# Optimization experiments

Measured on AMD Instinct MI355X. Metric: run time of the kernel, lower is better.

Reference implementation:

```python
import jax, jax.numpy as jnp
import numpy as np

# --- config constants (match init_kwargs) ---
TOP_K = 2          # num_experts_per_token
N_GROUP = 4        # num_expert_group
TOPK_GROUP = 2     # groups selected per token
SCALE = 2.5        # routed_scaling_factor
B, S, D = 2, 2048, 1024
E, F = 8, 512      # num_experts, moe_intermediate_size
SH = 1024          # shared intermediate = moe_intermediate_size * num_shared_experts


def setup_inputs() -> dict:
    key = jax.random.key(0)
    ks = jax.random.split(key, 10)
    w = 0.02
    return {
        "hidden_states": jax.random.normal(ks[0], (B, S, D), jnp.float32),
        "gate_w": jax.random.normal(ks[1], (E, D), jnp.float32) * w,
        "gate_bias": jax.random.normal(ks[2], (E,), jnp.float32) * 0.01,
        "w1": jax.random.normal(ks[3], (E, F, D), jnp.float32) * w,
        "w2": jax.random.normal(ks[4], (E, D, F), jnp.float32) * w,
        "w3": jax.random.normal(ks[5], (E, F, D), jnp.float32) * w,
        "shared_gate_w": jax.random.normal(ks[6], (SH, D), jnp.float32) * w,
        "shared_up_w": jax.random.normal(ks[7], (SH, D), jnp.float32) * w,
        "shared_down_w": jax.random.normal(ks[8], (D, SH), jnp.float32) * w,
    }


def _moe_gate(x2d, gate_w, gate_bias):
    """DeepSeek-V3 style group-limited sigmoid gate (inference path)."""
    T = x2d.shape[0]
    logits = x2d.astype(jnp.float32) @ gate_w.T.astype(jnp.float32)  # [T,E]
    scores = jax.nn.sigmoid(logits)
    sc = scores + gate_bias[None, :]                                  # e_score_correction_bias
    grp = sc.reshape(T, N_GROUP, E // N_GROUP)
    group_scores = jax.lax.top_k(grp, 2)[0].sum(-1)                   # [T,G] sum of top-2 in group
    gidx = jax.lax.top_k(group_scores, TOPK_GROUP)[1]                 # [T,topk_group]
    gmask = jnp.zeros((T, N_GROUP), sc.dtype).at[jnp.arange(T)[:, None], gidx].set(1.0)
    smask = jnp.repeat(gmask, E // N_GROUP, axis=1)                   # [T,E]
    tmp = jnp.where(smask > 0, sc, 0.0)                               # masked_fill(~mask, 0)
    tidx = jax.lax.top_k(tmp, TOP_K)[1]                               # [T,top_k]
    tw = jnp.take_along_axis(scores, tidx, axis=1)                    # weights from unbiased scores
    tw = tw / (tw.sum(-1, keepdims=True) + 1e-20)                     # moe_renormalize
    return tidx, tw * SCALE


def reference(hidden_states, gate_w, gate_bias, w1, w2, w3,
              shared_gate_w, shared_up_w, shared_down_w):
    b, s, d = hidden_states.shape
    x = hidden_states.reshape(-1, d)                                  # [T,D]
    T = x.shape[0]
    tidx, tw = _moe_gate(x, gate_w, gate_bias)
    # dense combine weights: ew[t,e] = sum_k tw[t,k] * (tidx[t,k]==e)
    ew = jnp.zeros((T, E), x.dtype).at[jnp.arange(T)[:, None], tidx].add(tw.astype(x.dtype))
    # routed experts (SwiGLU), computed per expert and combined with ew
    h = jax.nn.silu(jnp.einsum('td,efd->tef', x, w1)) * jnp.einsum('td,efd->tef', x, w3)
    y = jnp.einsum('tef,edf,te->td', h, w2, ew)
    # shared experts applied to identity
    shared = (jax.nn.silu(x @ shared_gate_w.T) * (x @ shared_up_w.T)) @ shared_down_w.T
    return (y + shared).reshape(b, s, d)
```

## Files before the change

kernel.cpp:

```cpp
#include <hip/hip_runtime.h>
#include <hip/hip_bf16.h>
#include <stdint.h>

#define T_TOK 4096
#define D_DIM 1024
#define E_NUM 8
#define F_DIM 512
#define SH_DIM 1024
#define SCALE_F 2.5f

#define BM 128
#define BN 128
#define BK 32
#define LDT 40

#define NBIG (E_NUM * F_DIM * D_DIM)
#define NSML (SH_DIM * D_DIM)
#define NCONV_CHUNKS ((3 * NBIG + 3 * NSML) / 4)
#define MAX_TILES 72

typedef unsigned short ushort_t;
typedef __attribute__((ext_vector_type(8))) short short8;
typedef __attribute__((ext_vector_type(4))) short short4v;
typedef __attribute__((ext_vector_type(4))) float f32x4;

__device__ inline ushort_t f2bf(float f) {
  union { float f; unsigned u; } cv; cv.f = f;
  unsigned u = cv.u;
  unsigned r = (u + 0x7FFFu + ((u >> 16) & 1u)) >> 16;
  return (ushort_t)r;
}

__global__ void gate_kernel(const float* __restrict__ x, const float* __restrict__ gw,
                            const float* __restrict__ gb, float* __restrict__ ew,
                            ushort_t* __restrict__ xb) {
  int t = blockIdx.x;
  int lane = threadIdx.x;
  const float* xr = x + (size_t)t * D_DIM;
  float xv[16];
#pragma unroll
  for (int i = 0; i < 16; i++) xv[i] = xr[lane + (i << 6)];
#pragma unroll
  for (int i = 0; i < 16; i++) xb[(size_t)t * D_DIM + lane + (i << 6)] = f2bf(xv[i]);
  float logit[E_NUM];
#pragma unroll
  for (int e = 0; e < E_NUM; e++) {
    const float* wr = gw + (size_t)e * D_DIM;
    float s = 0.f;
#pragma unroll
    for (int i = 0; i < 16; i++) s += xv[i] * wr[lane + (i << 6)];
#pragma unroll
    for (int off = 32; off; off >>= 1) s += __shfl_xor(s, off, 64);
    logit[e] = s;
  }
  if (lane == 0) {
    float scores[E_NUM], sc[E_NUM];
#pragma unroll
    for (int e = 0; e < E_NUM; e++) {
      scores[e] = 1.f / (1.f + expf(-logit[e]));
      sc[e] = scores[e] + gb[e];
    }
    float gs[4];
#pragma unroll
    for (int g = 0; g < 4; g++) gs[g] = sc[2 * g] + sc[2 * g + 1];
    int g0 = 0;
#pragma unroll
    for (int g = 1; g < 4; g++) if (gs[g] > gs[g0]) g0 = g;
    int g1 = -1;
#pragma unroll
    for (int g = 0; g < 4; g++) { if (g == g0) continue; if (g1 < 0 || gs[g] > gs[g1]) g1 = g; }
    float tmp[E_NUM];
#pragma unroll
    for (int e = 0; e < E_NUM; e++) {
      int g = e >> 1;
      tmp[e] = (g == g0 || g == g1) ? sc[e] : 0.f;
    }
    int e0 = 0;
#pragma unroll
    for (int e = 1; e < E_NUM; e++) if (tmp[e] > tmp[e0]) e0 = e;
    int e1 = -1;
#pragma unroll
    for (int e = 0; e < E_NUM; e++) { if (e == e0) continue; if (e1 < 0 || tmp[e] > tmp[e1]) e1 = e; }
    float w0 = scores[e0], w1v = scores[e1];
    float inv = SCALE_F / (w0 + w1v + 1e-20f);
    float o[E_NUM];
#pragma unroll
    for (int e = 0; e < E_NUM; e++) o[e] = 0.f;
    o[e0] = w0 * inv;
    o[e1] = w1v * inv;
#pragma unroll
    for (int e = 0; e < E_NUM; e++) ew[t * E_NUM + e] = o[e];
  }
}

__global__ void convert_kernel(const float* __restrict__ w1, const float* __restrict__ w2,
                               const float* __restrict__ w3, const float* __restrict__ sg,
                               const float* __restrict__ su, const float* __restrict__ sd,
                               ushort_t* __restrict__ w1b, ushort_t* __restrict__ w2b,
                               ushort_t* __restrict__ w3b, ushort_t* __restrict__ sgb,
                               ushort_t* __restrict__ sub, ushort_t* __restrict__ sdb) {
  size_t chunk = (size_t)blockIdx.x * blockDim.x + threadIdx.x;
  if (chunk >= (size_t)NCONV_CHUNKS) return;
  size_t idx = chunk * 4;
  const float* src; ushort_t* dst;
  if (idx < (size_t)NBIG)                    { src = w1; dst = w1b; }
  else if (idx < 2ull * NBIG)                { src = w2; dst = w2b; idx -= (size_t)NBIG; }
  else if (idx < 3ull * NBIG)                { src = w3; dst = w3b; idx -= 2ull * NBIG; }
  else if (idx < 3ull * NBIG + NSML)         { src = sg; dst = sgb; idx -= 3ull * NBIG; }
  else if (idx < 3ull * NBIG + 2ull * NSML)  { src = su; dst = sub; idx -= 3ull * NBIG + NSML; }
  else                                       { src = sd; dst = sdb; idx -= 3ull * NBIG + 2ull * NSML; }
  f32x4 v = *(const f32x4*)&src[idx];
  short4v o;
  o[0] = (short)f2bf(v[0]); o[1] = (short)f2bf(v[1]);
  o[2] = (short)f2bf(v[2]); o[3] = (short)f2bf(v[3]);
  *(short4v*)&dst[idx] = o;
}

__global__ void build_lists(const float* __restrict__ ew, int* __restrict__ counts,
                            int* __restrict__ toklist) {
  int t = blockIdx.x * blockDim.x + threadIdx.x;
  if (t >= T_TOK) return;
#pragma unroll
  for (int e = 0; e < E_NUM; e++) {
    if (ew[t * E_NUM + e] > 0.f) {
      int p = atomicAdd(&counts[e], 1);
      toklist[e * T_TOK + p] = t;
    }
  }
}

__global__ void assign_kernel(const int* __restrict__ counts, int4* __restrict__ assign,
                              int* __restrict__ meta) {
  if (threadIdx.x != 0 || blockIdx.x != 0) return;
  int total = 0, base = 0;
  for (int e = 0; e < E_NUM; e++) {
    int c = counts[e];
    int nt = (c + BM - 1) / BM;
    for (int i = 0; i < nt; i++) {
      assign[total] = make_int4(e, i, base, c);
      total++;
    }
    base += nt * BM;
  }
  meta[0] = total;
}

__global__ __launch_bounds__(256, 2)
void shared_gemm1(const ushort_t* __restrict__ xb, const ushort_t* __restrict__ gwb,
                  const ushort_t* __restrict__ uwb, ushort_t* __restrict__ hout) {
  __shared__ short la[BM * LDT], lb1[BN * LDT], lb2[BN * LDT];
  int tid = threadIdx.x, wid = tid >> 6, lane = tid & 63;
  int m0 = blockIdx.x * BM, n0 = blockIdx.y * BN;
  int wm = (wid >> 1) << 6, wn = (wid & 1) << 6;
  f32x4 acc1[4][4] = {{{0.f}}}, acc2[4][4] = {{{0.f}}};
  for (int k0 = 0; k0 < D_DIM; k0 += BK) {
#pragma unroll
    for (int i = tid; i < BM * 4; i += 256) {
      int r = i >> 2, c = (i & 3) << 3;
      *(short8*)&la[r * LDT + c]  = *(const short8*)&xb[(size_t)(m0 + r) * D_DIM + k0 + c];
      *(short8*)&lb1[r * LDT + c] = *(const short8*)&gwb[(size_t)(n0 + r) * D_DIM + k0 + c];
      *(short8*)&lb2[r * LDT + c] = *(const short8*)&uwb[(size_t)(n0 + r) * D_DIM + k0 + c];
    }
    __syncthreads();
    int rsel = lane & 15, ksel = (lane >> 4) << 3;
    short8 af[4], bf1[4], bf2[4];
#pragma unroll
    for (int i = 0; i < 4; i++) {
      af[i]  = *(const short8*)&la[(wm + i * 16 + rsel) * LDT + ksel];
      bf1[i] = *(const short8*)&lb1[(wn + i * 16 + rsel) * LDT + ksel];
      bf2[i] = *(const short8*)&lb2[(wn + i * 16 + rsel) * LDT + ksel];
    }
#pragma unroll
    for (int mi = 0; mi < 4; mi++)
#pragma unroll
      for (int ni = 0; ni < 4; ni++) {
        acc1[mi][ni] = __builtin_amdgcn_mfma_f32_16x16x32_bf16(af[mi], bf1[ni], acc1[mi][ni], 0, 0, 0);
        acc2[mi][ni] = __builtin_amdgcn_mfma_f32_16x16x32_bf16(af[mi], bf2[ni], acc2[mi][ni], 0, 0, 0);
      }
    __syncthreads();
  }
  int cw = lane & 15, rw = (lane >> 4) << 2;
#pragma unroll
  for (int mi = 0; mi < 4; mi++)
#pragma unroll
    for (int ni = 0; ni < 4; ni++)
#pragma unroll
      for (int r = 0; r < 4; r++) {
        int row = m0 + wm + mi * 16 + rw + r;
        int col = n0 + wn + ni * 16 + cw;
        float g = acc1[mi][ni][r], u = acc2[mi][ni][r];
        float h = g * (1.f / (1.f + __expf(-g))) * u;
        hout[(size_t)row * SH_DIM + col] = f2bf(h);
      }
}

__global__ __launch_bounds__(256, 2)
void shared_gemm2(const ushort_t* __restrict__ hb, const ushort_t* __restrict__ dwb,
                  float* __restrict__ out) {
  __shared__ short la[BM * LDT], lb[BN * LDT];
  int tid = threadIdx.x, wid = tid >> 6, lane = tid & 63;
  int m0 = blockIdx.x * BM, n0 = blockIdx.y * BN;
  int wm = (wid >> 1) << 6, wn = (wid & 1) << 6;
  f32x4 acc[4][4] = {{{0.f}}};
  for (int k0 = 0; k0 < SH_DIM; k0 += BK) {
#pragma unroll
    for (int i = tid; i < BM * 4; i += 256) {
      int r = i >> 2, c = (i & 3) << 3;
      *(short8*)&la[r * LDT + c] = *(const short8*)&hb[(size_t)(m0 + r) * SH_DIM + k0 + c];
      *(short8*)&lb[r * LDT + c] = *(const short8*)&dwb[(size_t)(n0 + r) * SH_DIM + k0 + c];
    }
    __syncthreads();
    int rsel = lane & 15, ksel = (lane >> 4) << 3;
    short8 af[4], bf[4];
#pragma unroll
    for (int i = 0; i < 4; i++) {
      af[i] = *(const short8*)&la[(wm + i * 16 + rsel) * LDT + ksel];
      bf[i] = *(const short8*)&lb[(wn + i * 16 + rsel) * LDT + ksel];
    }
#pragma unroll
    for (int mi = 0; mi < 4; mi++)
#pragma unroll
      for (int ni = 0; ni < 4; ni++)
        acc[mi][ni] = __builtin_amdgcn_mfma_f32_16x16x32_bf16(af[mi], bf[ni], acc[mi][ni], 0, 0, 0);
    __syncthreads();
  }
  int cw = lane & 15, rw = (lane >> 4) << 2;
#pragma unroll
  for (int mi = 0; mi < 4; mi++)
#pragma unroll
    for (int ni = 0; ni < 4; ni++)
#pragma unroll
      for (int r = 0; r < 4; r++) {
        int row = m0 + wm + mi * 16 + rw + r;
        int col = n0 + wn + ni * 16 + cw;
        out[(size_t)row * D_DIM + col] = acc[mi][ni][r];
      }
}

__global__ __launch_bounds__(256, 2)
void routed_gemm1(const ushort_t* __restrict__ xb, const ushort_t* __restrict__ w1b,
                  const ushort_t* __restrict__ w3b, const int* __restrict__ toklist,
                  const int4* __restrict__ assign, const int* __restrict__ meta,
                  ushort_t* __restrict__ hbuf) {
  if ((int)blockIdx.x >= meta[0]) return;
  int4 as = assign[blockIdx.x];
  int e = as.x, tile = as.y, sbase = as.z, cnt = as.w;
  int n0 = blockIdx.y * BN;
  __shared__ short la[BM * LDT], lb1[BN * LDT], lb2[BN * LDT];
  __shared__ int ttok[BM];
  int tid = threadIdx.x, wid = tid >> 6, lane = tid & 63;
  if (tid < BM) {
    int idx = tile * BM + tid;
    ttok[tid] = (idx < cnt) ? toklist[e * T_TOK + idx] : -1;
  }
  __syncthreads();
  int wm = (wid >> 1) << 6, wn = (wid & 1) << 6;
  f32x4 acc1[4][4] = {{{0.f}}}, acc2[4][4] = {{{0.f}}};
  for (int k0 = 0; k0 < D_DIM; k0 += BK) {
#pragma unroll
    for (int i = tid; i < BM * 4; i += 256) {
      int r = i >> 2, c = (i & 3) << 3;
      int tk = ttok[r];
      short8 va = {};
      if (tk >= 0) va = *(const short8*)&xb[(size_t)tk * D_DIM + k0 + c];
      *(short8*)&la[r * LDT + c] = va;
      *(short8*)&lb1[r * LDT + c] = *(const short8*)&w1b[((size_t)e * F_DIM + n0 + r) * D_DIM + k0 + c];
      *(short8*)&lb2[r * LDT + c] = *(const short8*)&w3b[((size_t)e * F_DIM + n0 + r) * D_DIM + k0 + c];
    }
    __syncthreads();
    int rsel = lane & 15, ksel = (lane >> 4) << 3;
    short8 af[4], bf1[4], bf2[4];
#pragma unroll
    for (int i = 0; i < 4; i++) {
      af[i]  = *(const short8*)&la[(wm + i * 16 + rsel) * LDT + ksel];
      bf1[i] = *(const short8*)&lb1[(wn + i * 16 + rsel) * LDT + ksel];
      bf2[i] = *(const short8*)&lb2[(wn + i * 16 + rsel) * LDT + ksel];
    }
#pragma unroll
    for (int mi = 0; mi < 4; mi++)
#pragma unroll
      for (int ni = 0; ni < 4; ni++) {
        acc1[mi][ni] = __builtin_amdgcn_mfma_f32_16x16x32_bf16(af[mi], bf1[ni], acc1[mi][ni], 0, 0, 0);
        acc2[mi][ni] = __builtin_amdgcn_mfma_f32_16x16x32_bf16(af[mi], bf2[ni], acc2[mi][ni], 0, 0, 0);
      }
    __syncthreads();
  }
  int cw = lane & 15, rw = (lane >> 4) << 2;
#pragma unroll
  for (int mi = 0; mi < 4; mi++)
#pragma unroll
    for (int ni = 0; ni < 4; ni++)
#pragma unroll
      for (int r = 0; r < 4; r++) {
        int lrow = wm + mi * 16 + rw + r;
        int col = n0 + wn + ni * 16 + cw;
        float g = acc1[mi][ni][r], u = acc2[mi][ni][r];
        float h = g * (1.f / (1.f + __expf(-g))) * u;
        hbuf[(size_t)(sbase + tile * BM + lrow) * F_DIM + col] = f2bf(h);
      }
}

__global__ __launch_bounds__(256, 2)
void routed_gemm2(const ushort_t* __restrict__ hbuf, const ushort_t* __restrict__ w2b,
                  const int* __restrict__ toklist, const float* __restrict__ ew,
                  const int4* __restrict__ assign, const int* __restrict__ meta,
                  float* __restrict__ out) {
  if ((int)blockIdx.x >= meta[0]) return;
  int4 as = assign[blockIdx.x];
  int e = as.x, tile = as.y, sbase = as.z, cnt = as.w;
  int n0 = blockIdx.y * BN;
  __shared__ short la[BM * LDT], lb[BN * LDT];
  __shared__ int ttok[BM];
  __shared__ float twt[BM];
  int tid = threadIdx.x, wid = tid >> 6, lane = tid & 63;
  if (tid < BM) {
    int idx = tile * BM + tid;
    int tk = (idx < cnt) ? toklist[e * T_TOK + idx] : -1;
    ttok[tid] = tk;
    twt[tid] = (tk >= 0) ? ew[tk * E_NUM + e] : 0.f;
  }
  __syncthreads();
  int wm = (wid >> 1) << 6, wn = (wid & 1) << 6;
  f32x4 acc[4][4] = {{{0.f}}};
  for (int k0 = 0; k0 < F_DIM; k0 += BK) {
#pragma unroll
    for (int i = tid; i < BM * 4; i += 256) {
      int r = i >> 2, c = (i & 3) << 3;
      *(short8*)&la[r * LDT + c] = *(const short8*)&hbuf[(size_t)(sbase + tile * BM + r) * F_DIM + k0 + c];
      *(short8*)&lb[r * LDT + c] = *(const short8*)&w2b[((size_t)e * D_DIM + n0 + r) * F_DIM + k0 + c];
    }
    __syncthreads();
    int rsel = lane & 15, ksel = (lane >> 4) << 3;
    short8 af[4], bf[4];
#pragma unroll
    for (int i = 0; i < 4; i++) {
      af[i] = *(const short8*)&la[(wm + i * 16 + rsel) * LDT + ksel];
      bf[i] = *(const short8*)&lb[(wn + i * 16 + rsel) * LDT + ksel];
    }
#pragma unroll
    for (int mi = 0; mi < 4; mi++)
#pragma unroll
      for (int ni = 0; ni < 4; ni++)
        acc[mi][ni] = __builtin_amdgcn_mfma_f32_16x16x32_bf16(af[mi], bf[ni], acc[mi][ni], 0, 0, 0);
    __syncthreads();
  }
  int cw = lane & 15, rw = (lane >> 4) << 2;
#pragma unroll
  for (int mi = 0; mi < 4; mi++)
#pragma unroll
    for (int ni = 0; ni < 4; ni++)
#pragma unroll
      for (int r = 0; r < 4; r++) {
        int lrow = wm + mi * 16 + rw + r;
        int tk = ttok[lrow];
        if (tk >= 0) {
          int col = n0 + wn + ni * 16 + cw;
          atomicAdd(&out[(size_t)tk * D_DIM + col], twt[lrow] * acc[mi][ni][r]);
        }
      }
}

extern "C" void kernel_launch(void* const* d_in, const int* in_sizes, int n_in,
                              void* d_out, int out_size, void* d_ws, size_t ws_size,
                              hipStream_t stream) {
  const float* x  = (const float*)d_in[0];
  const float* gw = (const float*)d_in[1];
  const float* gb = (const float*)d_in[2];
  const float* w1 = (const float*)d_in[3];
  const float* w2 = (const float*)d_in[4];
  const float* w3 = (const float*)d_in[5];
  const float* sg = (const float*)d_in[6];
  const float* su = (const float*)d_in[7];
  const float* sd = (const float*)d_in[8];
  float* out = (float*)d_out;

  char* ws = (char*)d_ws;
  size_t off = 0;
  auto alloc = [&](size_t bytes) {
    char* p = ws + off;
    off += (bytes + 255) & ~(size_t)255;
    return p;
  };
  ushort_t* xb   = (ushort_t*)alloc((size_t)T_TOK * D_DIM * 2);
  ushort_t* w1b  = (ushort_t*)alloc((size_t)NBIG * 2);
  ushort_t* w2b  = (ushort_t*)alloc((size_t)NBIG * 2);
  ushort_t* w3b  = (ushort_t*)alloc((size_t)NBIG * 2);
  ushort_t* sgb  = (ushort_t*)alloc((size_t)NSML * 2);
  ushort_t* sub  = (ushort_t*)alloc((size_t)NSML * 2);
  ushort_t* sdb  = (ushort_t*)alloc((size_t)NSML * 2);
  float*    ew   = (float*)alloc((size_t)T_TOK * E_NUM * 4);
  ushort_t* hsh  = (ushort_t*)alloc((size_t)T_TOK * SH_DIM * 2);
  ushort_t* hbuf = (ushort_t*)alloc((size_t)MAX_TILES * BM * F_DIM * 2);
  int*      toklist = (int*)alloc((size_t)E_NUM * T_TOK * 4);
  int*      counts  = (int*)alloc(64);
  int4*     assign  = (int4*)alloc((MAX_TILES + 8) * sizeof(int4));
  int*      meta    = (int*)alloc(64);

  hipMemsetAsync(counts, 0, 64, stream);
  gate_kernel<<<T_TOK, 64, 0, stream>>>(x, gw, gb, ew, xb);
  convert_kernel<<<NCONV_CHUNKS / 256, 256, 0, stream>>>(w1, w2, w3, sg, su, sd,
                                                         w1b, w2b, w3b, sgb, sub, sdb);
  build_lists<<<(T_TOK + 255) / 256, 256, 0, stream>>>(ew, counts, toklist);
  assign_kernel<<<1, 64, 0, stream>>>(counts, assign, meta);
  shared_gemm1<<<dim3(T_TOK / BM, SH_DIM / BN), 256, 0, stream>>>(xb, sgb, sub, hsh);
  shared_gemm2<<<dim3(T_TOK / BM, D_DIM / BN), 256, 0, stream>>>(hsh, sdb, out);
  routed_gemm1<<<dim3(MAX_TILES, F_DIM / BN), 256, 0, stream>>>(xb, w1b, w3b, toklist,
                                                                assign, meta, hbuf);
  routed_gemm2<<<dim3(MAX_TILES, D_DIM / BN), 256, 0, stream>>>(hbuf, w2b, toklist, ew,
                                                                assign, meta, out);
}
```

Baseline: 310.8 us.

## Merge shared and routed expert GEMMs into grouped up and down launches

Combines the shared-expert and routed-expert up-projection GEMMs into one launch, and likewise the two down-projection GEMMs, with block IDs split between the shared and routed work. This lets shared and routed tiles run together on the GPU, filling compute units that the small routed grid left idle and removing launch gaps. Since both kinds of block now accumulate into the output, the output is zeroed with a memset and the shared path goes through the weighted accumulate epilogue, which adds extra memory traffic and atomics.

```diff
diff --git a/kernel.cpp b/kernel.cpp
--- a/kernel.cpp
+++ b/kernel.cpp
@@ -18,6 +18,11 @@
 #define NSML (SH_DIM * D_DIM)
 #define NCONV_CHUNKS ((3 * NBIG + 3 * NSML) / 4)
 #define MAX_TILES 72
+
+#define UP_SHARED_BLOCKS 256
+#define UP_TOTAL (UP_SHARED_BLOCKS + MAX_TILES * 4)
+#define DN_SHARED_BLOCKS 256
+#define DN_TOTAL (DN_SHARED_BLOCKS + MAX_TILES * 8)
 
 typedef unsigned short ushort_t;
 typedef __attribute__((ext_vector_type(8))) short short8;
@@ -146,20 +151,58 @@
 }
 
 __global__ __launch_bounds__(256, 2)
-void shared_gemm1(const ushort_t* __restrict__ xb, const ushort_t* __restrict__ gwb,
-                  const ushort_t* __restrict__ uwb, ushort_t* __restrict__ hout) {
+void up_gemm(const ushort_t* __restrict__ xb,
+             const ushort_t* __restrict__ sgb, const ushort_t* __restrict__ sub,
+             const ushort_t* __restrict__ w1b, const ushort_t* __restrict__ w3b,
+             const int* __restrict__ toklist,
+             const int4* __restrict__ assign, const int* __restrict__ meta,
+             ushort_t* __restrict__ hsh, ushort_t* __restrict__ hbuf) {
   __shared__ short la[BM * LDT], lb1[BN * LDT], lb2[BN * LDT];
+  __shared__ int ttok[BM];
+  int bid = blockIdx.x;
   int tid = threadIdx.x, wid = tid >> 6, lane = tid & 63;
-  int m0 = blockIdx.x * BM, n0 = blockIdx.y * BN;
+
+  const ushort_t *b1base, *b2base;
+  ushort_t* dst;
+  int n0, dstride;
+  size_t rowbase;
+
+  if (bid < UP_SHARED_BLOCKS) {
+    int m0 = (bid >> 3) * BM;
+    n0 = (bid & 7) * BN;
+    b1base = sgb + (size_t)n0 * D_DIM;
+    b2base = sub + (size_t)n0 * D_DIM;
+    dst = hsh; dstride = SH_DIM; rowbase = m0;
+    if (tid < BM) ttok[tid] = m0 + tid;
+  } else {
+    int rid = bid - UP_SHARED_BLOCKS;
+    int tidx = rid >> 2;
+    if (tidx >= meta[0]) return;
+    int4 as = assign[tidx];
+    int e = as.x, tile = as.y, sbase = as.z, cnt = as.w;
+    n0 = (rid & 3) * BN;
+    b1base = w1b + ((size_t)e * F_DIM + n0) * D_DIM;
+    b2base = w3b + ((size_t)e * F_DIM + n0) * D_DIM;
+    dst = hbuf; dstride = F_DIM; rowbase = (size_t)sbase + (size_t)tile * BM;
+    if (tid < BM) {
+      int idx = tile * BM + tid;
+      ttok[tid] = (idx < cnt) ? toklist[e * T_TOK + idx] : -1;
+    }
+  }
+  __syncthreads();
+
   int wm = (wid >> 1) << 6, wn = (wid & 1) << 6;
   f32x4 acc1[4][4] = {{{0.f}}}, acc2[4][4] = {{{0.f}}};
   for (int k0 = 0; k0 < D_DIM; k0 += BK) {
 #pragma unroll
     for (int i = tid; i < BM * 4; i += 256) {
       int r = i >> 2, c = (i & 3) << 3;
-      *(short8*)&la[r * LDT + c]  = *(const short8*)&xb[(size_t)(m0 + r) * D_DIM + k0 + c];
-      *(short8*)&lb1[r * LDT + c] = *(const short8*)&gwb[(size_t)(n0 + r) * D_DIM + k0 + c];
-      *(short8*)&lb2[r * LDT + c] = *(const short8*)&uwb[(size_t)(n0 + r) * D_DIM + k0 + c];
+      int tk = ttok[r];
+      short8 va = {};
+      if (tk >= 0) va = *(const short8*)&xb[(size_t)tk * D_DIM + k0 + c];
+      *(short8*)&la[r * LDT + c]  = va;
+      *(short8*)&lb1[r * LDT + c] = *(const short8*)&b1base[(size_t)r * D_DIM + k0 + c];
+      *(short8*)&lb2[r * LDT + c] = *(const short8*)&b2base[(size_t)r * D_DIM + k0 + c];
     }
     __syncthreads();
     int rsel = lane & 15, ksel = (lane >> 4) << 3;
@@ -186,148 +229,63 @@
     for (int ni = 0; ni < 4; ni++)
 #pragma unroll
       for (int r = 0; r < 4; r++) {
-        int row = m0 + wm + mi * 16 + rw + r;
-        int col = n0 + wn + ni * 16 + cw;
-        float g = acc1[mi][ni][r], u = acc2[mi][ni][r];
-        float h = g * (1.f / (1.f + __expf(-g))) * u;
-        hout[(size_t)row * SH_DIM + col] = f2bf(h);
-      }
-}
-
-__global__ __launch_bounds__(256, 2)
-void shared_gemm2(const ushort_t* __restrict__ hb, const ushort_t* __restrict__ dwb,
-                  float* __restrict__ out) {
-  __shared__ short la[BM * LDT], lb[BN * LDT];
-  int tid = threadIdx.x, wid = tid >> 6, lane = tid & 63;
-  int m0 = blockIdx.x * BM, n0 = blockIdx.y * BN;
-  int wm = (wid >> 1) << 6, wn = (wid & 1) << 6;
-  f32x4 acc[4][4] = {{{0.f}}};
-  for (int k0 = 0; k0 < SH_DIM; k0 += BK) {
-#pragma unroll
-    for (int i = tid; i < BM * 4; i += 256) {
-      int r = i >> 2, c = (i & 3) << 3;
-      *(short8*)&la[r * LDT + c] = *(const short8*)&hb[(size_t)(m0 + r) * SH_DIM + k0 + c];
-      *(short8*)&lb[r * LDT + c] = *(const short8*)&dwb[(size_t)(n0 + r) * SH_DIM + k0 + c];
-    }
-    __syncthreads();
-    int rsel = lane & 15, ksel = (lane >> 4) << 3;
-    short8 af[4], bf[4];
-#pragma unroll
-    for (int i = 0; i < 4; i++) {
-      af[i] = *(const short8*)&la[(wm + i * 16 + rsel) * LDT + ksel];
-      bf[i] = *(const short8*)&lb[(wn + i * 16 + rsel) * LDT + ksel];
-    }
-#pragma unroll
-    for (int mi = 0; mi < 4; mi++)
-#pragma unroll
-      for (int ni = 0; ni < 4; ni++)
-        acc[mi][ni] = __builtin_amdgcn_mfma_f32_16x16x32_bf16(af[mi], bf[ni], acc[mi][ni], 0, 0, 0);
-    __syncthreads();
-  }
-  int cw = lane & 15, rw = (lane >> 4) << 2;
-#pragma unroll
-  for (int mi = 0; mi < 4; mi++)
-#pragma unroll
-    for (int ni = 0; ni < 4; ni++)
-#pragma unroll
-      for (int r = 0; r < 4; r++) {
-        int row = m0 + wm + mi * 16 + rw + r;
-        int col = n0 + wn + ni * 16 + cw;
-        out[(size_t)row * D_DIM + col] = acc[mi][ni][r];
-      }
-}
-
-__global__ __launch_bounds__(256, 2)
-void routed_gemm1(const ushort_t* __restrict__ xb, const ushort_t* __restrict__ w1b,
-                  const ushort_t* __restrict__ w3b, const int* __restrict__ toklist,
-                  const int4* __restrict__ assign, const int* __restrict__ meta,
-                  ushort_t* __restrict__ hbuf) {
-  if ((int)blockIdx.x >= meta[0]) return;
-  int4 as = assign[blockIdx.x];
-  int e = as.x, tile = as.y, sbase = as.z, cnt = as.w;
-  int n0 = blockIdx.y * BN;
-  __shared__ short la[BM * LDT], lb1[BN * LDT], lb2[BN * LDT];
-  __shared__ int ttok[BM];
-  int tid = threadIdx.x, wid = tid >> 6, lane = tid & 63;
-  if (tid < BM) {
-    int idx = tile * BM + tid;
-    ttok[tid] = (idx < cnt) ? toklist[e * T_TOK + idx] : -1;
-  }
-  __syncthreads();
-  int wm = (wid >> 1) << 6, wn = (wid & 1) << 6;
-  f32x4 acc1[4][4] = {{{0.f}}}, acc2[4][4] = {{{0.f}}};
-  for (int k0 = 0; k0 < D_DIM; k0 += BK) {
-#pragma unroll
-    for (int i = tid; i < BM * 4; i += 256) {
-      int r = i >> 2, c = (i & 3) << 3;
-      int tk = ttok[r];
-      short8 va = {};
-      if (tk >= 0) va = *(const short8*)&xb[(size_t)tk * D_DIM + k0 + c];
-      *(short8*)&la[r * LDT + c] = va;
-      *(short8*)&lb1[r * LDT + c] = *(const short8*)&w1b[((size_t)e * F_DIM + n0 + r) * D_DIM + k0 + c];
-      *(short8*)&lb2[r * LDT + c] = *(const short8*)&w3b[((size_t)e * F_DIM + n0 + r) * D_DIM + k0 + c];
-    }
-    __syncthreads();
-    int rsel = lane & 15, ksel = (lane >> 4) << 3;
-    short8 af[4], bf1[4], bf2[4];
-#pragma unroll
-    for (int i = 0; i < 4; i++) {
-      af[i]  = *(const short8*)&la[(wm + i * 16 + rsel) * LDT + ksel];
-      bf1[i] = *(const short8*)&lb1[(wn + i * 16 + rsel) * LDT + ksel];
-      bf2[i] = *(const short8*)&lb2[(wn + i * 16 + rsel) * LDT + ksel];
-    }
-#pragma unroll
-    for (int mi = 0; mi < 4; mi++)
-#pragma unroll
-      for (int ni = 0; ni < 4; ni++) {
-        acc1[mi][ni] = __builtin_amdgcn_mfma_f32_16x16x32_bf16(af[mi], bf1[ni], acc1[mi][ni], 0, 0, 0);
-        acc2[mi][ni] = __builtin_amdgcn_mfma_f32_16x16x32_bf16(af[mi], bf2[ni], acc2[mi][ni], 0, 0, 0);
-      }
-    __syncthreads();
-  }
-  int cw = lane & 15, rw = (lane >> 4) << 2;
-#pragma unroll
-  for (int mi = 0; mi < 4; mi++)
-#pragma unroll
-    for (int ni = 0; ni < 4; ni++)
-#pragma unroll
-      for (int r = 0; r < 4; r++) {
         int lrow = wm + mi * 16 + rw + r;
         int col = n0 + wn + ni * 16 + cw;
         float g = acc1[mi][ni][r], u = acc2[mi][ni][r];
         float h = g * (1.f / (1.f + __expf(-g))) * u;
-        hbuf[(size_t)(sbase + tile * BM + lrow) * F_DIM + col] = f2bf(h);
+        dst[(rowbase + lrow) * (size_t)dstride + col] = f2bf(h);
       }
 }
 
 __global__ __launch_bounds__(256, 2)
-void routed_gemm2(const ushort_t* __restrict__ hbuf, const ushort_t* __restrict__ w2b,
-                  const int* __restrict__ toklist, const float* __restrict__ ew,
-                  const int4* __restrict__ assign, const int* __restrict__ meta,
-                  float* __restrict__ out) {
-  if ((int)blockIdx.x >= meta[0]) return;
-  int4 as = assign[blockIdx.x];
-  int e = as.x, tile = as.y, sbase = as.z, cnt = as.w;
-  int n0 = blockIdx.y * BN;
+void down_gemm(const ushort_t* __restrict__ hsh, const ushort_t* __restrict__ hbuf,
+               const ushort_t* __restrict__ sdb, const ushort_t* __restrict__ w2b,
+               const int* __restrict__ toklist, const float* __restrict__ ew,
+               const int4* __restrict__ assign, const int* __restrict__ meta,
+               float* __restrict__ out) {
   __shared__ short la[BM * LDT], lb[BN * LDT];
   __shared__ int ttok[BM];
   __shared__ float twt[BM];
+  int bid = blockIdx.x;
   int tid = threadIdx.x, wid = tid >> 6, lane = tid & 63;
-  if (tid < BM) {
-    int idx = tile * BM + tid;
-    int tk = (idx < cnt) ? toklist[e * T_TOK + idx] : -1;
-    ttok[tid] = tk;
-    twt[tid] = (tk >= 0) ? ew[tk * E_NUM + e] : 0.f;
+
+  const ushort_t *abase, *bbase;
+  int n0, kend;
+
+  if (bid < DN_SHARED_BLOCKS) {
+    int m0 = (bid >> 3) * BM;
+    n0 = (bid & 7) * BN;
+    abase = hsh + (size_t)m0 * SH_DIM;
+    bbase = sdb + (size_t)n0 * SH_DIM;
+    kend = SH_DIM;
+    if (tid < BM) { ttok[tid] = m0 + tid; twt[tid] = 1.f; }
+  } else {
+    int rid = bid - DN_SHARED_BLOCKS;
+    int tidx = rid >> 3;
+    if (tidx >= meta[0]) return;
+    int4 as = assign[tidx];
+    int e = as.x, tile = as.y, sbase = as.z, cnt = as.w;
+    n0 = (rid & 7) * BN;
+    abase = hbuf + ((size_t)sbase + (size_t)tile * BM) * F_DIM;
+    bbase = w2b + ((size_t)e * D_DIM + n0) * F_DIM;
+    kend = F_DIM;
+    if (tid < BM) {
+      int idx = tile * BM + tid;
+      int tk = (idx < cnt) ? toklist[e * T_TOK + idx] : -1;
+      ttok[tid] = tk;
+      twt[tid] = (tk >= 0) ? ew[tk * E_NUM + e] : 0.f;
+    }
   }
   __syncthreads();
+
   int wm = (wid >> 1) << 6, wn = (wid & 1) << 6;
   f32x4 acc[4][4] = {{{0.f}}};
-  for (int k0 = 0; k0 < F_DIM; k0 += BK) {
+  for (int k0 = 0; k0 < kend; k0 += BK) {
 #pragma unroll
     for (int i = tid; i < BM * 4; i += 256) {
       int r = i >> 2, c = (i & 3) << 3;
-      *(short8*)&la[r * LDT + c] = *(const short8*)&hbuf[(size_t)(sbase + tile * BM + r) * F_DIM + k0 + c];
-      *(short8*)&lb[r * LDT + c] = *(const short8*)&w2b[((size_t)e * D_DIM + n0 + r) * F_DIM + k0 + c];
+      *(short8*)&la[r * LDT + c] = *(const short8*)&abase[(size_t)r * kend + k0 + c];
+      *(short8*)&lb[r * LDT + c] = *(const short8*)&bbase[(size_t)r * kend + k0 + c];
     }
     __syncthreads();
     int rsel = lane & 15, ksel = (lane >> 4) << 3;
@@ -397,15 +355,14 @@
   int*      meta    = (int*)alloc(64);
 
   hipMemsetAsync(counts, 0, 64, stream);
+  hipMemsetAsync(out, 0, (size_t)out_size * sizeof(float), stream);
   gate_kernel<<<T_TOK, 64, 0, stream>>>(x, gw, gb, ew, xb);
   convert_kernel<<<NCONV_CHUNKS / 256, 256, 0, stream>>>(w1, w2, w3, sg, su, sd,
                                                          w1b, w2b, w3b, sgb, sub, sdb);
   build_lists<<<(T_TOK + 255) / 256, 256, 0, stream>>>(ew, counts, toklist);
   assign_kernel<<<1, 64, 0, stream>>>(counts, assign, meta);
-  shared_gemm1<<<dim3(T_TOK / BM, SH_DIM / BN), 256, 0, stream>>>(xb, sgb, sub, hsh);
-  shared_gemm2<<<dim3(T_TOK / BM, D_DIM / BN), 256, 0, stream>>>(hsh, sdb, out);
-  routed_gemm1<<<dim3(MAX_TILES, F_DIM / BN), 256, 0, stream>>>(xb, w1b, w3b, toklist,
-                                                                assign, meta, hbuf);
-  routed_gemm2<<<dim3(MAX_TILES, D_DIM / BN), 256, 0, stream>>>(hbuf, w2b, toklist, ew,
-                                                                assign, meta, out);
-}
+  up_gemm<<<UP_TOTAL, 256, 0, stream>>>(xb, sgb, sub, w1b, w3b, toklist, assign, meta,
+                                        hsh, hbuf);
+  down_gemm<<<DN_TOTAL, 256, 0, stream>>>(hsh, hbuf, sdb, w2b, toklist, ew, assign, meta,
+                                          out);
+}
```

Result: faster. 300.5 us (-3.3%).
